# Optimization experiments

Measured on AMD Instinct MI355X. Metric: run time of the kernel, lower is better.

The kernel has to match this reference:

```python
import jax, jax.numpy as jnp
import numpy as np

BETA = 0.9
THRESHOLD = 1.0
SLOPE = 25.0


def _heaviside(x):
    return (x > 0).astype(x.dtype)


def setup_inputs() -> dict:
    key = jax.random.key(0)
    k = jax.random.split(key, 5)
    B, T, I, H, C = 256, 500, 256, 512, 8
    x = jax.random.normal(k[0], (B, T, I), dtype=jnp.float32)
    W1 = jax.random.normal(k[1], (H, I), dtype=jnp.float32) * (1.0 / np.sqrt(I))
    b1 = jax.random.normal(k[2], (H,), dtype=jnp.float32) * 0.01
    W2 = jax.random.normal(k[3], (C, H), dtype=jnp.float32) * (1.0 / np.sqrt(H))
    b2 = jax.random.normal(k[4], (C,), dtype=jnp.float32) * 0.01
    return {"x": x, "W1": W1, "b1": b1, "W2": W2, "b2": b2}


def reference(x, W1, b1, W2, b2):
    # x: (B, T, I)
    B, T, I = x.shape
    # Time-invariant fc1 batched outside the recurrence: (B, T, H)
    cur1 = jnp.einsum('bti,hi->bth', x, W1) + b1
    cur1_t = jnp.swapaxes(cur1, 0, 1)  # (T, B, H)

    def step(mem, cur):
        # snntorch Leaky (reset_mechanism='subtract'):
        # reset computed from previous mem crossing threshold
        reset = _heaviside(mem - THRESHOLD)
        mem_new = BETA * mem + cur - reset * THRESHOLD
        spk = _heaviside(mem_new - THRESHOLD)
        return mem_new, spk

    mem0 = jnp.zeros((B, W1.shape[0]), dtype=x.dtype)
    _, spks = jax.lax.scan(step, mem0, cur1_t)  # spks: (T, B, H)

    # out_sum = sum_t (spk_t @ W2^T + b2) = (sum_t spk_t) @ W2^T + T*b2
    spk_sum = spks.sum(axis=0)  # (B, H)
    out_sum = spk_sum @ W2.T + jnp.asarray(T, x.dtype) * b2  # (B, C)
    return out_sum
```

## Files before the change

kernel.cpp:

```cpp
#include <hip/hip_runtime.h>


#define B_   256
#define T_   500
#define I_   256
#define H_   512
#define C_   8

#define TC   128
#define BK   32
#define NKS  8
#define NCH  4
#define NR   (NCH * NKS)

#define WBUF  0
#define XBUF0 32768
#define XBUF1 49152

typedef __attribute__((ext_vector_type(8))) _Float16 half8;
typedef __attribute__((ext_vector_type(2))) __fp16 f16x2;
typedef __attribute__((ext_vector_type(4))) float f32x4;

typedef __attribute__((address_space(1))) const unsigned int as1_uint;
typedef __attribute__((address_space(3))) unsigned int as3_uint;

__device__ __forceinline__ void lds_dma16(const void* g, void* l) {
  __builtin_amdgcn_global_load_lds((as1_uint*)g, (as3_uint*)l, 16, 0, 0);
}

#define MFMA16(A, B, Cc) __builtin_amdgcn_mfma_f32_16x16x32_f16(A, B, Cc, 0, 0, 0)

__global__ void init_out_kernel(const float* __restrict__ b2,
                                float* __restrict__ out) {
  int idx = blockIdx.x * 256 + threadIdx.x;
  if (idx < B_ * C_) out[idx] = (float)T_ * b2[idx & (C_ - 1)];
}

__global__ void split_w1_kernel(const float* __restrict__ W1,
                                char* __restrict__ ws) {
  const int n = blockIdx.x * 256 + threadIdx.x;
  if (n >= H_ * NKS * 4) return;
  const int blk = n >> 10, r = n & 1023;
  const int ks = blk >> 1, hh = blk & 1;
  const int h = hh * 256 + (r >> 8) * 64 + ((r >> 6) & 3) * 16 + (r & 15);
  const int c = (r >> 4) & 3;
  const float* src = W1 + h * I_ + ks * BK + c * 8;
  union { half8 v; _Float16 e[8]; } hi, lo;
  #pragma unroll
  for (int e = 0; e < 8; ++e) {
    const float w = 16.0f * src[e];
    const _Float16 wh = (_Float16)w;
    hi.e[e] = wh;
    lo.e[e] = (_Float16)(w - (float)wh);
  }
  char* dst = ws + (size_t)blk * 32768 + (size_t)r * 16;
  *(half8*)dst = hi.v;
  *(half8*)(dst + 16384) = lo.v;
}

__device__ __forceinline__ void load_x8(const float* xb, int t, int col,
                                        float* a) {
  if (t < T_) {
    const float* p = xb + (size_t)t * I_ + col;
    const float4 v0 = *(const float4*)p;
    const float4 v1 = *(const float4*)(p + 4);
    a[0] = v0.x; a[1] = v0.y; a[2] = v0.z; a[3] = v0.w;
    a[4] = v1.x; a[5] = v1.y; a[6] = v1.z; a[7] = v1.w;
  } else {
    #pragma unroll
    for (int e = 0; e < 8; ++e) a[e] = 0.f;
  }
}

__device__ __forceinline__ void cvt_store(char* base, int tt, int l,
                                          const float* a) {
  union { half8 v; f16x2 p[4]; } h8, l8;
  #pragma unroll
  for (int k = 0; k < 4; ++k) {
    const f16x2 ha = __builtin_amdgcn_cvt_pkrtz(a[2 * k], a[2 * k + 1]);
    h8.p[k] = ha;
    l8.p[k] = __builtin_amdgcn_cvt_pkrtz(a[2 * k] - (float)ha[0],
                                         a[2 * k + 1] - (float)ha[1]);
  }
  *(half8*)(base + tt * 1024 + l * 16) = h8.v;
  *(half8*)(base + 8192 + tt * 1024 + l * 16) = l8.v;
}

__global__ __launch_bounds__(256, 2) void snn_mfma3(
    const float* __restrict__ x, const char* __restrict__ ws,
    const float* __restrict__ b1, const float* __restrict__ W2,
    float* __restrict__ out) {
  __shared__ __align__(16) char smem[65536];

  const int tid = threadIdx.x;
  const int b = blockIdx.x, hf = blockIdx.y;
  const int l = tid & 63, wv = tid >> 6;

  const float* xb = x + (size_t)b * (T_ * I_);

  const int xrow = l & 15;
  const int xcolb = (l >> 4) * 8;

  float biasj[4];
  #pragma unroll
  for (int j = 0; j < 4; ++j)
    biasj[j] = 16.0f * b1[hf * 256 + wv * 64 + j * 16 + (l & 15)];

  float mreg = 0.f, cnt = 0.f;
  bool sp = false;

  f32x4 acc[8][4];
  #pragma unroll
  for (int i = 0; i < 8; ++i)
    #pragma unroll
    for (int j = 0; j < 4; ++j)
      acc[i][j] = (f32x4){biasj[j], biasj[j], biasj[j], biasj[j]};

  {
    const char* wg = ws + (size_t)hf * 32768;
    #pragma unroll
    for (int q = 0; q < 4; ++q) {
      const int o = (q * 256 + tid) * 16;
      lds_dma16(wg + o, smem + WBUF + o);
      lds_dma16(wg + 16384 + o, smem + WBUF + 16384 + o);
    }
    float a8[2][8];
    load_x8(xb, 2 * wv * 16 + xrow, xcolb, a8[0]);
    load_x8(xb, (2 * wv + 1) * 16 + xrow, xcolb, a8[1]);
    cvt_store(smem + XBUF0, 2 * wv, l, a8[0]);
    cvt_store(smem + XBUF0, 2 * wv + 1, l, a8[1]);
    __syncthreads();
  }

  #pragma unroll 1
  for (int r = 0; r < NR; ++r) {
    const int ks = r & 7;
    const int xcur = XBUF0 + (r & 1) * 16384;
    const int xnxt = XBUF0 + ((r + 1) & 1) * 16384;
    const bool do_stage = (r + 1 < NR);

    float a8[2][8];
    if (do_stage) {
      const int t1 = ((r + 1) >> 3) * TC, c1 = ((r + 1) & 7) * BK + xcolb;
      load_x8(xb, t1 + 2 * wv * 16 + xrow, c1, a8[0]);
      load_x8(xb, t1 + (2 * wv + 1) * 16 + xrow, c1, a8[1]);
    }

    half8 ah[8], al[8], bh[4], bl[4];
    #pragma unroll
    for (int i = 0; i < 8; ++i) {
      ah[i] = *(const half8*)(smem + xcur + i * 1024 + (l << 4));
      al[i] = *(const half8*)(smem + xcur + 8192 + i * 1024 + (l << 4));
    }
    #pragma unroll
    for (int j = 0; j < 4; ++j) {
      bh[j] = *(const half8*)(smem + WBUF + (wv << 12) + (j << 10) + (l << 4));
      bl[j] = *(const half8*)(smem + WBUF + 16384 + (wv << 12) + (j << 10) +
                              (l << 4));
    }
    #pragma unroll
    for (int i = 0; i < 8; ++i)
      #pragma unroll
      for (int j = 0; j < 4; ++j) {
        acc[i][j] = MFMA16(ah[i], bh[j], acc[i][j]);
        acc[i][j] = MFMA16(al[i], bh[j], acc[i][j]);
        acc[i][j] = MFMA16(ah[i], bl[j], acc[i][j]);
      }

    if (ks == 7) {
      asm volatile("" ::: "memory");
      const int t0 = (r >> 3) * TC;
      char* dw = smem + xnxt + (wv << 12);
      #pragma unroll
      for (int p = 0; p < 8; ++p) {
        #pragma unroll
        for (int j = 0; j < 4; ++j)
          *(f32x4*)(dw + ((l >> 4) << 10) + (((j << 4) + (l & 15)) << 4)) =
              acc[p][j];
        const int tb = t0 + p * 16;
        #pragma unroll
        for (int g = 0; g < 4; ++g) {
          const float4 v = *(const float4*)(dw + (g << 10) + (l << 4));
          const float cv[4] = {v.x, v.y, v.z, v.w};
          #pragma unroll
          for (int e = 0; e < 4; ++e) {
            if (tb + g * 4 + e < T_) {
              const float rst = sp ? 16.0f : 0.0f;
              mreg = fmaf(0.9f, mreg, cv[e]) - rst;
              sp = mreg > 16.0f;
              if (sp) cnt += 1.0f;
            }
          }
        }
      }
      #pragma unroll
      for (int i = 0; i < 8; ++i)
        #pragma unroll
        for (int j = 0; j < 4; ++j)
          acc[i][j] = (f32x4){biasj[j], biasj[j], biasj[j], biasj[j]};
    }

    __syncthreads();

    if (do_stage) {
      const char* wg = ws + (size_t)((((r + 1) & 7) << 1) + hf) * 32768;
      #pragma unroll
      for (int q = 0; q < 4; ++q) {
        const int o = (q * 256 + tid) * 16;
        lds_dma16(wg + o, smem + WBUF + o);
        lds_dma16(wg + 16384 + o, smem + WBUF + 16384 + o);
      }
      cvt_store(smem + xnxt, 2 * wv, l, a8[0]);
      cvt_store(smem + xnxt, 2 * wv + 1, l, a8[1]);
    }
    __syncthreads();
  }

  const int hglob = hf * 256 + wv * 64 + l;
  #pragma unroll
  for (int c = 0; c < C_; ++c) {
    float p = cnt * W2[c * H_ + hglob];
    #pragma unroll
    for (int m = 32; m >= 1; m >>= 1) p += __shfl_xor(p, m, 64);
    if (l == 0) atomicAdd(&out[b * C_ + c], p);
  }
}

extern "C" void kernel_launch(void* const* d_in, const int* in_sizes, int n_in,
                              void* d_out, int out_size, void* d_ws,
                              size_t ws_size, hipStream_t stream) {
  (void)in_sizes; (void)n_in; (void)ws_size; (void)out_size;
  const float* x  = (const float*)d_in[0];
  const float* W1 = (const float*)d_in[1];
  const float* b1 = (const float*)d_in[2];
  const float* W2 = (const float*)d_in[3];
  const float* b2 = (const float*)d_in[4];
  float* out = (float*)d_out;
  char* ws = (char*)d_ws;

  init_out_kernel<<<dim3((B_ * C_ + 255) / 256), dim3(256), 0, stream>>>(b2, out);
  split_w1_kernel<<<dim3(H_ * NKS * 4 / 256), dim3(256), 0, stream>>>(W1, ws);
  snn_mfma3<<<dim3(B_, 2), dim3(256), 0, stream>>>(x, ws, b1, W2, out);
}
```

Baseline: 249.6 us.

## Keep x fragments in registers and double-buffer W1 in LDS with one barrier

Time chunk shrinks from 128 to 64 steps. Each wave now converts its own x fragments straight into registers instead of staging them through LDS, and LDS holds two W1 buffers filled by async DMA, so one s_barrier per iteration replaces two __syncthreads. The aim is to cut LDS traffic and synchronisation stalls and to overlap the W1 load with MFMA work. In exchange, each wave loads x for all 64 timesteps itself, duplicating x global loads across the four waves. The reduced scan output is written into the current W1 buffer, and the barrier before memory-counter waits on the DMA is removed, which risks races.

```diff
diff --git a/kernel.cpp b/kernel.cpp
--- a/kernel.cpp
+++ b/kernel.cpp
@@ -7,15 +7,11 @@
 #define H_   512
 #define C_   8
 
-#define TC   128
+#define TC   64
 #define BK   32
 #define NKS  8
-#define NCH  4
+#define NCH  8
 #define NR   (NCH * NKS)
-
-#define WBUF  0
-#define XBUF0 32768
-#define XBUF1 49152
 
 typedef __attribute__((ext_vector_type(8))) _Float16 half8;
 typedef __attribute__((ext_vector_type(2))) __fp16 f16x2;
@@ -29,6 +25,7 @@
 }
 
 #define MFMA16(A, B, Cc) __builtin_amdgcn_mfma_f32_16x16x32_f16(A, B, Cc, 0, 0, 0)
+#define SB0() __builtin_amdgcn_sched_barrier(0)
 
 __global__ void init_out_kernel(const float* __restrict__ b2,
                                 float* __restrict__ out) {
@@ -72,21 +69,20 @@
   }
 }
 
-__device__ __forceinline__ void cvt_store(char* base, int tt, int l,
-                                          const float* a) {
-  union { half8 v; f16x2 p[4]; } h8, l8;
+__device__ __forceinline__ void cvt_frag(const float* a, half8& hh, half8& ll) {
+  union { half8 v; f16x2 p[4]; } H, L;
   #pragma unroll
   for (int k = 0; k < 4; ++k) {
     const f16x2 ha = __builtin_amdgcn_cvt_pkrtz(a[2 * k], a[2 * k + 1]);
-    h8.p[k] = ha;
-    l8.p[k] = __builtin_amdgcn_cvt_pkrtz(a[2 * k] - (float)ha[0],
-                                         a[2 * k + 1] - (float)ha[1]);
-  }
-  *(half8*)(base + tt * 1024 + l * 16) = h8.v;
-  *(half8*)(base + 8192 + tt * 1024 + l * 16) = l8.v;
-}
-
-__global__ __launch_bounds__(256, 2) void snn_mfma3(
+    H.p[k] = ha;
+    L.p[k] = __builtin_amdgcn_cvt_pkrtz(a[2 * k] - (float)ha[0],
+                                        a[2 * k + 1] - (float)ha[1]);
+  }
+  hh = H.v;
+  ll = L.v;
+}
+
+__global__ __launch_bounds__(256, 2) void snn_mfma4(
     const float* __restrict__ x, const char* __restrict__ ws,
     const float* __restrict__ b1, const float* __restrict__ W2,
     float* __restrict__ out) {
@@ -95,12 +91,11 @@
   const int tid = threadIdx.x;
   const int b = blockIdx.x, hf = blockIdx.y;
   const int l = tid & 63, wv = tid >> 6;
-
-  const float* xb = x + (size_t)b * (T_ * I_);
-
   const int xrow = l & 15;
   const int xcolb = (l >> 4) * 8;
 
+  const float* xb = x + (size_t)b * (T_ * I_);
+
   float biasj[4];
   #pragma unroll
   for (int j = 0; j < 4; ++j)
@@ -109,70 +104,74 @@
   float mreg = 0.f, cnt = 0.f;
   bool sp = false;
 
-  f32x4 acc[8][4];
-  #pragma unroll
-  for (int i = 0; i < 8; ++i)
+  f32x4 acc[4][4];
+  #pragma unroll
+  for (int i = 0; i < 4; ++i)
     #pragma unroll
     for (int j = 0; j < 4; ++j)
       acc[i][j] = (f32x4){biasj[j], biasj[j], biasj[j], biasj[j]};
 
+  half8 ah[4], al[4];
+
   {
     const char* wg = ws + (size_t)hf * 32768;
     #pragma unroll
-    for (int q = 0; q < 4; ++q) {
+    for (int q = 0; q < 8; ++q) {
       const int o = (q * 256 + tid) * 16;
-      lds_dma16(wg + o, smem + WBUF + o);
-      lds_dma16(wg + 16384 + o, smem + WBUF + 16384 + o);
-    }
-    float a8[2][8];
-    load_x8(xb, 2 * wv * 16 + xrow, xcolb, a8[0]);
-    load_x8(xb, (2 * wv + 1) * 16 + xrow, xcolb, a8[1]);
-    cvt_store(smem + XBUF0, 2 * wv, l, a8[0]);
-    cvt_store(smem + XBUF0, 2 * wv + 1, l, a8[1]);
-    __syncthreads();
+      lds_dma16(wg + o, smem + o);
+    }
+    float raw[4][8];
+    #pragma unroll
+    for (int i = 0; i < 4; ++i) load_x8(xb, i * 16 + xrow, xcolb, raw[i]);
+    #pragma unroll
+    for (int i = 0; i < 4; ++i) cvt_frag(raw[i], ah[i], al[i]);
+    SB0();
+    __builtin_amdgcn_s_barrier();
   }
 
   #pragma unroll 1
   for (int r = 0; r < NR; ++r) {
-    const int ks = r & 7;
-    const int xcur = XBUF0 + (r & 1) * 16384;
-    const int xnxt = XBUF0 + ((r + 1) & 1) * 16384;
-    const bool do_stage = (r + 1 < NR);
-
-    float a8[2][8];
-    if (do_stage) {
-      const int t1 = ((r + 1) >> 3) * TC, c1 = ((r + 1) & 7) * BK + xcolb;
-      load_x8(xb, t1 + 2 * wv * 16 + xrow, c1, a8[0]);
-      load_x8(xb, t1 + (2 * wv + 1) * 16 + xrow, c1, a8[1]);
-    }
-
-    half8 ah[8], al[8], bh[4], bl[4];
-    #pragma unroll
-    for (int i = 0; i < 8; ++i) {
-      ah[i] = *(const half8*)(smem + xcur + i * 1024 + (l << 4));
-      al[i] = *(const half8*)(smem + xcur + 8192 + i * 1024 + (l << 4));
-    }
+    const char* wb = smem + (r & 1) * 32768;
+    const bool stage = (r + 1 < NR);
+    float raw[4][8];
+
+    if (stage) {
+      const int r1 = r + 1;
+      const char* wg = ws + (size_t)(((r1 & 7) << 1) + hf) * 32768;
+      char* wdst = smem + (r1 & 1) * 32768;
+      #pragma unroll
+      for (int q = 0; q < 8; ++q) {
+        const int o = (q * 256 + tid) * 16;
+        lds_dma16(wg + o, wdst + o);
+      }
+      const int t1 = (r1 >> 3) * TC, c1 = (r1 & 7) * BK + xcolb;
+      #pragma unroll
+      for (int i = 0; i < 4; ++i)
+        load_x8(xb, t1 + i * 16 + xrow, c1, raw[i]);
+    }
+    SB0();
+
+    half8 bh[4], bl[4];
     #pragma unroll
     for (int j = 0; j < 4; ++j) {
-      bh[j] = *(const half8*)(smem + WBUF + (wv << 12) + (j << 10) + (l << 4));
-      bl[j] = *(const half8*)(smem + WBUF + 16384 + (wv << 12) + (j << 10) +
-                              (l << 4));
-    }
-    #pragma unroll
-    for (int i = 0; i < 8; ++i)
+      bh[j] = *(const half8*)(wb + (wv << 12) + (j << 10) + (l << 4));
+      bl[j] = *(const half8*)(wb + 16384 + (wv << 12) + (j << 10) + (l << 4));
+    }
+    #pragma unroll
+    for (int i = 0; i < 4; ++i)
       #pragma unroll
       for (int j = 0; j < 4; ++j) {
         acc[i][j] = MFMA16(ah[i], bh[j], acc[i][j]);
         acc[i][j] = MFMA16(al[i], bh[j], acc[i][j]);
         acc[i][j] = MFMA16(ah[i], bl[j], acc[i][j]);
       }
-
-    if (ks == 7) {
-      asm volatile("" ::: "memory");
+    SB0();
+
+    if ((r & 7) == 7) {
+      char* dw = (char*)wb + (wv << 12);
       const int t0 = (r >> 3) * TC;
-      char* dw = smem + xnxt + (wv << 12);
-      #pragma unroll
-      for (int p = 0; p < 8; ++p) {
+      #pragma unroll
+      for (int p = 0; p < 4; ++p) {
         #pragma unroll
         for (int j = 0; j < 4; ++j)
           *(f32x4*)(dw + ((l >> 4) << 10) + (((j << 4) + (l & 15)) << 4)) =
@@ -194,26 +193,20 @@
         }
       }
       #pragma unroll
-      for (int i = 0; i < 8; ++i)
+      for (int i = 0; i < 4; ++i)
         #pragma unroll
         for (int j = 0; j < 4; ++j)
           acc[i][j] = (f32x4){biasj[j], biasj[j], biasj[j], biasj[j]};
     }
-
-    __syncthreads();
-
-    if (do_stage) {
-      const char* wg = ws + (size_t)((((r + 1) & 7) << 1) + hf) * 32768;
-      #pragma unroll
-      for (int q = 0; q < 4; ++q) {
-        const int o = (q * 256 + tid) * 16;
-        lds_dma16(wg + o, smem + WBUF + o);
-        lds_dma16(wg + 16384 + o, smem + WBUF + 16384 + o);
-      }
-      cvt_store(smem + xnxt, 2 * wv, l, a8[0]);
-      cvt_store(smem + xnxt, 2 * wv + 1, l, a8[1]);
-    }
-    __syncthreads();
+    SB0();
+
+    if (stage) {
+      #pragma unroll
+      for (int i = 0; i < 4; ++i) cvt_frag(raw[i], ah[i], al[i]);
+    }
+    SB0();
+
+    if (stage) __builtin_amdgcn_s_barrier();
   }
 
   const int hglob = hf * 256 + wv * 64 + l;
@@ -240,5 +233,5 @@
 
   init_out_kernel<<<dim3((B_ * C_ + 255) / 256), dim3(256), 0, stream>>>(b2, out);
   split_w1_kernel<<<dim3(H_ * NKS * 4 / 256), dim3(256), 0, stream>>>(W1, ws);
-  snn_mfma3<<<dim3(B_, 2), dim3(256), 0, stream>>>(x, ws, b1, W2, out);
-}
+  snn_mfma4<<<dim3(B_, 2), dim3(256), 0, stream>>>(x, ws, b1, W2, out);
+}
```

New measurement: 327.1 us. 1.31x slower.
